# Optimization experiments

Hardware: AMD Instinct MI355X
Metric: run time of the kernel (lower is better)

Reference implementation:

```python
import jax, jax.numpy as jnp
import numpy as np

NFRAMES = 8
N_ITERS = 32        # fixed-iteration Riemannian gradient descent (geomstats FrechetMean equivalent)
EPS = 1e-7


def _l2norm(x, axis=-1):
    return x / jnp.maximum(jnp.linalg.norm(x, axis=axis, keepdims=True), EPS)


def _frechet_mean_sphere(X):
    """Batched Frechet mean on the unit hypersphere.
    X: [..., n, d] unit vectors. Returns [..., d] unit mean.
    Iteration: mu <- Exp_mu( mean_i Log_mu(x_i) ).
    """
    mu0 = _l2norm(jnp.mean(X, axis=-2))

    def step(mu, _):
        dots = jnp.clip(jnp.einsum('...d,...kd->...k', mu, X), -1.0 + 1e-6, 1.0 - 1e-6)
        theta = jnp.arccos(dots)
        safe = theta > 1e-4
        coef = jnp.where(safe, theta / jnp.sin(jnp.where(safe, theta, 1.0)), 1.0)
        # Log map: [..., n, d]
        logs = coef[..., None] * (X - dots[..., None] * mu[..., None, :])
        v = jnp.mean(logs, axis=-2)                      # tangent mean [..., d]
        vn = jnp.linalg.norm(v, axis=-1, keepdims=True)
        vsafe = vn > 1e-9
        sinc = jnp.where(vsafe, jnp.sin(vn) / jnp.where(vsafe, vn, 1.0), 1.0)
        mu_new = jnp.cos(vn) * mu + sinc * v             # Exp map
        return _l2norm(mu_new), None

    mu, _ = jax.lax.scan(step, mu0, None, length=N_ITERS)
    return mu


def setup_inputs() -> dict:
    key = jax.random.key(0)
    k1, k2 = jax.random.split(key)
    support_vecs = jax.random.normal(k1, (25, 64, NFRAMES * 2048), dtype=jnp.float32)
    target_vec = jax.random.normal(k2, (64, NFRAMES * 2048), dtype=jnp.float32)
    return {"support_vecs": support_vecs, "target_vec": target_vec}


def reference(support_vecs, target_vec):
    seqlen, bs, df = support_vecs.shape
    sup = _l2norm(support_vecs.reshape(seqlen, bs, NFRAMES, -1))   # [s,b,n,2048]
    tgt = _l2norm(target_vec.reshape(bs, NFRAMES, -1))             # [b,n,2048]
    support_means = _frechet_mean_sphere(sup)                      # [s,b,2048]
    target_means = _frechet_mean_sphere(tgt)                       # [b,2048]
    similarities = jnp.einsum('sbd,bd->sb', support_means, target_means)
    return similarities
```

## Files before the change

kernel.cpp:

```cpp
#include <hip/hip_runtime.h>
#include <math.h>

#define NFR 8
#define DD 2048
#define NS 25
#define NB 64
#define NPAIR (NS*NB)
#define NITER 32
#define WS_TGT 320000
#define SOLVE_BLKS 100

typedef __attribute__((ext_vector_type(8))) short short8;
typedef __attribute__((ext_vector_type(4))) float f32x4;

__device__ __forceinline__ float acos_fast(float x) {
    const float ax = fabsf(x);
    const bool big = ax > 0.5f;
    const float z = big ? 0.5f * (1.f - ax) : x * x;
    const float s = big ? sqrtf(z) : ax;
    float p = fmaf(z, 4.2163199048e-2f, 2.4181311049e-2f);
    p = fmaf(z, p, 4.5470025998e-2f);
    p = fmaf(z, p, 7.4953002686e-2f);
    p = fmaf(z, p, 1.6666752422e-1f);
    const float asin_s = fmaf(s * z, p, s);
    const float asin_abs = big ? (1.5707963267948966f - 2.f * asin_s) : asin_s;
    return 1.5707963267948966f - copysignf(asin_abs, x);
}

#define SPLIT2(a, b, HI, LO) { \
    const float ha_ = __uint_as_float(__float_as_uint(a) & 0xFFFF0000u); \
    const float hb_ = __uint_as_float(__float_as_uint(b) & 0xFFFF0000u); \
    HI = __builtin_amdgcn_perm(__float_as_uint(b), __float_as_uint(a), 0x07060302u); \
    LO = __builtin_amdgcn_perm(__float_as_uint((b) - hb_), __float_as_uint((a) - ha_), 0x07060302u); \
}

__device__ __forceinline__ void load_lds16(const float* g, float* l) {
    __builtin_amdgcn_global_load_lds(
        (const __attribute__((address_space(1))) void*)g,
        (__attribute__((address_space(3))) void*)l, 16, 0, 0);
}

__global__ __launch_bounds__(512) void gram_kernel(const float* __restrict__ sup,
                                                   const float* __restrict__ tgt,
                                                   float* __restrict__ ws) {
    const int bid = blockIdx.x;
    const int xcd = bid & 7;
    const int q   = bid >> 3;
    const int b   = xcd * 8 + (q & 7);
    const int sq  = q >> 3;
    const int s   = sq % NS;
    const int kh  = sq / NS;
    const int p   = s * NB + b;
    const int tid = threadIdx.x;
    const int wv  = tid >> 6;
    const int l   = tid & 63;
    const int row = l & 15;
    const int kg  = l >> 4;

    __shared__ float lds[16384];

    #pragma unroll
    for (int i = 0; i < 2; ++i) {
        const int r  = 2 * wv + i;
        const int r7 = r & 7;
        const float* g = (r < 8)
            ? sup + ((size_t)p * NFR + r) * DD + kh * 1024
            : tgt + ((size_t)b * NFR + (r - 8)) * DD + kh * 1024;
        const float* gl = g + (size_t)((l ^ r7) * 4);
        float* d = lds + r * 1024;
        #pragma unroll
        for (int c = 0; c < 4; ++c)
            load_lds16(gl + c * 256, d + c * 256);
    }
    __syncthreads();

    f32x4 accA = {0.f, 0.f, 0.f, 0.f};
    f32x4 accB = {0.f, 0.f, 0.f, 0.f};
    const int swz = (row & 7) << 4;
    const char* rowbase = (const char*)lds + row * 4096;
    #pragma unroll
    for (int st = 0; st < 4; ++st) {
        const int o0 = (wv * 128 + st * 32) * 4 + kg * 32;
        const float4 f0 = *(const float4*)(rowbase + (o0 ^ swz));
        const float4 f1 = *(const float4*)(rowbase + ((o0 + 16) ^ swz));
        union { unsigned int u[4]; short8 s8; } H, L;
        SPLIT2(f0.x, f0.y, H.u[0], L.u[0]);
        SPLIT2(f0.z, f0.w, H.u[1], L.u[1]);
        SPLIT2(f1.x, f1.y, H.u[2], L.u[2]);
        SPLIT2(f1.z, f1.w, H.u[3], L.u[3]);
        accA = __builtin_amdgcn_mfma_f32_16x16x32_bf16(H.s8, H.s8, accA, 0, 0, 0);
        accB = __builtin_amdgcn_mfma_f32_16x16x32_bf16(H.s8, L.s8, accB, 0, 0, 0);
        accB = __builtin_amdgcn_mfma_f32_16x16x32_bf16(L.s8, H.s8, accB, 0, 0, 0);
    }
    __syncthreads();

    float* part = lds;
    #pragma unroll
    for (int r = 0; r < 4; ++r)
        part[wv * 272 + (kg * 4 + r) * 17 + row] = accA[r] + accB[r];
    __syncthreads();

    if (tid < 256) {
        const int rr = tid >> 4, cc = tid & 15;
        float v = 0.f;
        #pragma unroll
        for (int w = 0; w < 8; ++w) v += part[w * 272 + rr * 17 + cc];
        if (rr < 8) {
            if (cc >= 8)
                ws[(size_t)(p * 2 + kh) * 100 + 36 + rr * 8 + (cc - 8)] = v;
            else if (cc >= rr)
                ws[(size_t)(p * 2 + kh) * 100 + rr * 8 + cc - rr * (rr + 1) / 2] = v;
        } else if (s == 0 && cc >= rr) {
            const int i8 = rr - 8, j8 = cc - 8;
            ws[WS_TGT + (size_t)(b * 2 + kh) * 36 + i8 * 8 + j8 - i8 * (i8 + 1) / 2] = v;
        }
    }
}

__global__ __launch_bounds__(256) void solve_kernel(const float* __restrict__ ws,
                                                    float* __restrict__ out) {
    const int bid = blockIdx.x;
    const int tid = threadIdx.x;
    __shared__ float synth[16 * 256];

    for (int e = tid; e < 4096; e += 256) {
        const int pp = e >> 8, ij = e & 255;
        const int i = ij >> 4, j = ij & 15;
        const int p = bid * 16 + pp;
        const int b = p & (NB - 1);
        float v = 0.f;
        if (i < 8) {
            if (j < 8) {
                const int ii = i < j ? i : j, jj = i < j ? j : i;
                const int t36 = ii*8 + jj - ii*(ii+1)/2;
                v = ws[(size_t)(p*2+0)*100 + t36] + ws[(size_t)(p*2+1)*100 + t36];
            } else {
                const int c64 = 36 + i*8 + (j-8);
                v = ws[(size_t)(p*2+0)*100 + c64] + ws[(size_t)(p*2+1)*100 + c64];
            }
        } else if (j >= 8) {
            const int i8 = i - 8, j8 = j - 8;
            const int ii = i8 < j8 ? i8 : j8, jj = i8 < j8 ? j8 : i8;
            const int t36 = ii*8 + jj - ii*(ii+1)/2;
            v = ws[WS_TGT + (size_t)(b*2+0)*36 + t36] + ws[WS_TGT + (size_t)(b*2+1)*36 + t36];
        }
        synth[e] = v;
    }
    __syncthreads();

    const int pp = tid >> 4;
    const int t16 = tid & 15;
    const int p = bid * 16 + pp;
    const float* graw = synth + pp * 256;
    const int j = t16 & 7;
    const int base = t16 & 8;
    const int R = base + j;
    const int cb = base;

    const float invn_own = rsqrtf(fmaxf(graw[R * 16 + R], 1e-14f));
    float Grow[8];
    #pragma unroll
    for (int k = 0; k < 8; ++k) {
        const float invk = rsqrtf(fmaxf(graw[(cb + k) * 16 + (cb + k)], 1e-14f));
        Grow[k] = graw[R * 16 + cb + k] * invn_own * invk;
    }

    float rs = 0.f;
    #pragma unroll
    for (int k = 0; k < 8; ++k) rs += Grow[k];
    rs += __shfl_xor(rs, 1, 8);
    rs += __shfl_xor(rs, 2, 8);
    rs += __shfl_xor(rs, 4, 8);
    float a_own = rsqrtf(fmaxf(rs, 6.4e-13f));
    float aAll[8];
    #pragma unroll
    for (int k = 0; k < 8; ++k) aAll[k] = a_own;

    for (int it = 0; it < NITER; ++it) {
        float dot = 0.f;
        #pragma unroll
        for (int k = 0; k < 8; ++k) dot = fmaf(Grow[k], aAll[k], dot);
        dot = fminf(fmaxf(dot, -1.f + 1e-6f), 1.f - 1e-6f);
        const float theta = acos_fast(dot);
        const float q = fmaf(-dot, dot, 1.0f);
        const float coef = (theta > 1e-4f) ? theta * rsqrtf(q) : 1.f;
        const float w = 0.125f * coef;
        float wAll[8];
        #pragma unroll
        for (int k = 0; k < 8; ++k) wAll[k] = __shfl(w, base + k, 16);
        float Gw = 0.f;
        #pragma unroll
        for (int k = 0; k < 8; ++k) Gw = fmaf(Grow[k], wAll[k], Gw);
        float u1 = a_own * Gw, u2 = w * Gw;
        u1 += __shfl_xor(u1, 1, 8);  u2 += __shfl_xor(u2, 1, 8);
        u1 += __shfl_xor(u1, 2, 8);  u2 += __shfl_xor(u2, 2, 8);
        u1 += __shfl_xor(u1, 4, 8);  u2 += __shfl_xor(u2, 4, 8);
        const float cdavg = u1;
        const float vnsq = fmaxf(u2 - cdavg * cdavg, 0.f);
        const float vn = sqrtf(vnsq);
        const float rev = vn * 0.15915494309189535f;
        const float sinv = __builtin_amdgcn_sinf(rev);
        const float cosv = __builtin_amdgcn_cosf(rev);
        const float sinc = (vn > 1e-9f) ? sinv / vn : 1.f;
        const float cn2 = fmaf(sinc * sinc, vnsq, cosv * cosv);
        const float rn = rsqrtf(fmaxf(cn2, 1e-14f));
        a_own = (cosv * a_own + sinc * fmaf(-cdavg, a_own, w)) * rn;
        #pragma unroll
        for (int k = 0; k < 8; ++k)
            aAll[k] = (cosv * aAll[k] + sinc * fmaf(-cdavg, aAll[k], wAll[k])) * rn;
    }

    const float ahat = a_own * invn_own;
    float at[8];
    #pragma unroll
    for (int q2 = 0; q2 < 8; ++q2) at[q2] = __shfl(ahat, 8 + q2, 16);
    float tacc = 0.f;
    #pragma unroll
    for (int q2 = 0; q2 < 8; ++q2) tacc = fmaf(graw[j * 16 + 8 + q2], at[q2], tacc);
    float sim = ahat * tacc;
    sim += __shfl_xor(sim, 1, 8);
    sim += __shfl_xor(sim, 2, 8);
    sim += __shfl_xor(sim, 4, 8);
    if (t16 == 0) out[p] = sim;
}

extern "C" void kernel_launch(void* const* d_in, const int* in_sizes, int n_in,
                              void* d_out, int out_size, void* d_ws, size_t ws_size,
                              hipStream_t stream) {
    const float* sup = (const float*)d_in[0];
    const float* tgt = (const float*)d_in[1];
    float* ws = (float*)d_ws;
    float* out = (float*)d_out;
    gram_kernel<<<NPAIR * 2, 512, 0, stream>>>(sup, tgt, ws);
    solve_kernel<<<SOLVE_BLKS, 256, 0, stream>>>(ws, out);
}
```

Measured before the change: 53.10 us.

## Pipeline support loads across seqlen slices with triple-buffered LDS in gram kernel

```diff
diff --git a/kernel.cpp b/kernel.cpp
--- a/kernel.cpp
+++ b/kernel.cpp
@@ -7,7 +7,7 @@
 #define NB 64
 #define NPAIR (NS*NB)
 #define NITER 32
-#define WS_TGT 320000
+#define WS_TGT 640000
 #define SOLVE_BLKS 100
 
 typedef __attribute__((ext_vector_type(8))) short short8;
@@ -44,76 +44,101 @@
                                                    const float* __restrict__ tgt,
                                                    float* __restrict__ ws) {
     const int bid = blockIdx.x;
-    const int xcd = bid & 7;
-    const int q   = bid >> 3;
-    const int b   = xcd * 8 + (q & 7);
-    const int sq  = q >> 3;
-    const int s   = sq % NS;
-    const int kh  = sq / NS;
-    const int p   = s * NB + b;
+    const int u   = bid >> 3;
+    const int b   = (bid & 7) * 8 + (u & 7);
+    const int u2  = u >> 3;
+    const int kq  = u2 & 3;
+    const int sg  = u2 >> 2;
     const int tid = threadIdx.x;
     const int wv  = tid >> 6;
     const int l   = tid & 63;
-    const int row = l & 15;
+    const int fr  = l & 15;
     const int kg  = l >> 4;
 
-    __shared__ float lds[16384];
-
-    #pragma unroll
-    for (int i = 0; i < 2; ++i) {
-        const int r  = 2 * wv + i;
-        const int r7 = r & 7;
-        const float* g = (r < 8)
-            ? sup + ((size_t)p * NFR + r) * DD + kh * 1024
-            : tgt + ((size_t)b * NFR + (r - 8)) * DD + kh * 1024;
-        const float* gl = g + (size_t)((l ^ r7) * 4);
-        float* d = lds + r * 1024;
-        #pragma unroll
-        for (int c = 0; c < 4; ++c)
-            load_lds16(gl + c * 256, d + c * 256);
-    }
-    __syncthreads();
-
-    f32x4 accA = {0.f, 0.f, 0.f, 0.f};
-    f32x4 accB = {0.f, 0.f, 0.f, 0.f};
-    const int swz = (row & 7) << 4;
-    const char* rowbase = (const char*)lds + row * 4096;
-    #pragma unroll
-    for (int st = 0; st < 4; ++st) {
-        const int o0 = (wv * 128 + st * 32) * 4 + kg * 32;
-        const float4 f0 = *(const float4*)(rowbase + (o0 ^ swz));
-        const float4 f1 = *(const float4*)(rowbase + ((o0 + 16) ^ swz));
-        union { unsigned int u[4]; short8 s8; } H, L;
-        SPLIT2(f0.x, f0.y, H.u[0], L.u[0]);
-        SPLIT2(f0.z, f0.w, H.u[1], L.u[1]);
-        SPLIT2(f1.x, f1.y, H.u[2], L.u[2]);
-        SPLIT2(f1.z, f1.w, H.u[3], L.u[3]);
-        accA = __builtin_amdgcn_mfma_f32_16x16x32_bf16(H.s8, H.s8, accA, 0, 0, 0);
-        accB = __builtin_amdgcn_mfma_f32_16x16x32_bf16(H.s8, L.s8, accB, 0, 0, 0);
-        accB = __builtin_amdgcn_mfma_f32_16x16x32_bf16(L.s8, H.s8, accB, 0, 0, 0);
-    }
-    __syncthreads();
-
-    float* part = lds;
-    #pragma unroll
-    for (int r = 0; r < 4; ++r)
-        part[wv * 272 + (kg * 4 + r) * 17 + row] = accA[r] + accB[r];
-    __syncthreads();
-
-    if (tid < 256) {
-        const int rr = tid >> 4, cc = tid & 15;
-        float v = 0.f;
-        #pragma unroll
-        for (int w = 0; w < 8; ++w) v += part[w * 272 + rr * 17 + cc];
-        if (rr < 8) {
-            if (cc >= 8)
-                ws[(size_t)(p * 2 + kh) * 100 + 36 + rr * 8 + (cc - 8)] = v;
-            else if (cc >= rr)
-                ws[(size_t)(p * 2 + kh) * 100 + rr * 8 + cc - rr * (rr + 1) / 2] = v;
-        } else if (s == 0 && cc >= rr) {
-            const int i8 = rr - 8, j8 = cc - 8;
-            ws[WS_TGT + (size_t)(b * 2 + kh) * 36 + i8 * 8 + j8 - i8 * (i8 + 1) / 2] = v;
-        }
+    __shared__ float tbuf[8 * 512];
+    __shared__ float sbuf[3][8 * 512];
+    __shared__ float part[8 * 272];
+
+    {
+        const float* g = tgt + ((size_t)b * NFR + wv) * DD + kq * 512;
+        const float* gl = g + (l ^ wv) * 4;
+        load_lds16(gl,       tbuf + wv * 512);
+        load_lds16(gl + 256, tbuf + wv * 512 + 256);
+    }
+    const int s0 = sg * 5;
+    {
+        #pragma unroll
+        for (int i = 0; i < 2; ++i) {
+            const float* g = sup + (((size_t)(s0 + i) * NB + b) * NFR + wv) * DD + kq * 512;
+            const float* gl = g + (l ^ wv) * 4;
+            load_lds16(gl,       sbuf[i] + wv * 512);
+            load_lds16(gl + 256, sbuf[i] + wv * 512 + 256);
+        }
+    }
+
+    #pragma unroll
+    for (int i = 0; i < 5; ++i) {
+        if (i + 2 <= 4) {
+            const int sl = (i + 2) % 3;
+            const float* g = sup + (((size_t)(s0 + i + 2) * NB + b) * NFR + wv) * DD + kq * 512;
+            const float* gl = g + (l ^ wv) * 4;
+            load_lds16(gl,       sbuf[sl] + wv * 512);
+            load_lds16(gl + 256, sbuf[sl] + wv * 512 + 256);
+        }
+        if (i <= 2)      asm volatile("s_waitcnt vmcnt(4)" ::: "memory");
+        else if (i == 3) asm volatile("s_waitcnt vmcnt(2)" ::: "memory");
+        else             asm volatile("s_waitcnt vmcnt(0)" ::: "memory");
+        __builtin_amdgcn_s_barrier();
+        __builtin_amdgcn_sched_barrier(0);
+
+        f32x4 accA = {0.f, 0.f, 0.f, 0.f};
+        f32x4 accB = {0.f, 0.f, 0.f, 0.f};
+        const char* rb = (const char*)((fr < 8) ? (sbuf[i % 3] + fr * 512)
+                                                : (tbuf + (fr - 8) * 512));
+        const int swz = (fr & 7) << 4;
+        #pragma unroll
+        for (int ch = 0; ch < 2; ++ch) {
+            const int o  = wv * 256 + ch * 128 + kg * 32;
+            const int oa = (o & 0xC00) | ((o & 0x3FF) ^ swz);
+            const int ob = ((o + 16) & 0xC00) | (((o + 16) & 0x3FF) ^ swz);
+            const float4 f0 = *(const float4*)(rb + oa);
+            const float4 f1 = *(const float4*)(rb + ob);
+            union { unsigned int u[4]; short8 s8; } H, L;
+            SPLIT2(f0.x, f0.y, H.u[0], L.u[0]);
+            SPLIT2(f0.z, f0.w, H.u[1], L.u[1]);
+            SPLIT2(f1.x, f1.y, H.u[2], L.u[2]);
+            SPLIT2(f1.z, f1.w, H.u[3], L.u[3]);
+            accA = __builtin_amdgcn_mfma_f32_16x16x32_bf16(H.s8, H.s8, accA, 0, 0, 0);
+            accB = __builtin_amdgcn_mfma_f32_16x16x32_bf16(H.s8, L.s8, accB, 0, 0, 0);
+            accB = __builtin_amdgcn_mfma_f32_16x16x32_bf16(L.s8, H.s8, accB, 0, 0, 0);
+        }
+
+        #pragma unroll
+        for (int r = 0; r < 4; ++r)
+            part[wv * 272 + (kg * 4 + r) * 17 + fr] = accA[r] + accB[r];
+        asm volatile("s_waitcnt lgkmcnt(0)" ::: "memory");
+        __builtin_amdgcn_s_barrier();
+        __builtin_amdgcn_sched_barrier(0);
+
+        if (tid < 256) {
+            const int rr = tid >> 4, cc = tid & 15;
+            float v = 0.f;
+            #pragma unroll
+            for (int w = 0; w < 8; ++w) v += part[w * 272 + rr * 17 + cc];
+            const size_t p4 = (size_t)(((s0 + i) * NB + b) * 4 + kq);
+            if (rr < 8) {
+                if (cc >= 8)
+                    ws[p4 * 100 + 36 + rr * 8 + (cc - 8)] = v;
+                else if (cc >= rr)
+                    ws[p4 * 100 + rr * 8 + cc - rr * (rr + 1) / 2] = v;
+            } else if (sg == 0 && i == 0 && cc >= rr) {
+                const int i8 = rr - 8, j8 = cc - 8;
+                ws[WS_TGT + (size_t)(b * 4 + kq) * 36 + i8 * 8 + j8 - i8 * (i8 + 1) / 2] = v;
+            }
+        }
+        asm volatile("s_waitcnt lgkmcnt(0)" ::: "memory");
+        __builtin_amdgcn_s_barrier();
+        __builtin_amdgcn_sched_barrier(0);
     }
 }
 
@@ -133,16 +158,18 @@
             if (j < 8) {
                 const int ii = i < j ? i : j, jj = i < j ? j : i;
                 const int t36 = ii*8 + jj - ii*(ii+1)/2;
-                v = ws[(size_t)(p*2+0)*100 + t36] + ws[(size_t)(p*2+1)*100 + t36];
+                #pragma unroll
+                for (int kq = 0; kq < 4; ++kq) v += ws[(size_t)(p*4+kq)*100 + t36];
             } else {
-                const int c64 = 36 + i*8 + (j-8);
-                v = ws[(size_t)(p*2+0)*100 + c64] + ws[(size_t)(p*2+1)*100 + c64];
+                #pragma unroll
+                for (int kq = 0; kq < 4; ++kq) v += ws[(size_t)(p*4+kq)*100 + 36 + i*8 + (j-8)];
             }
         } else if (j >= 8) {
             const int i8 = i - 8, j8 = j - 8;
             const int ii = i8 < j8 ? i8 : j8, jj = i8 < j8 ? j8 : i8;
             const int t36 = ii*8 + jj - ii*(ii+1)/2;
-            v = ws[WS_TGT + (size_t)(b*2+0)*36 + t36] + ws[WS_TGT + (size_t)(b*2+1)*36 + t36];
+            #pragma unroll
+            for (int kq = 0; kq < 4; ++kq) v += ws[WS_TGT + (size_t)(b*4+kq)*36 + t36];
         }
         synth[e] = v;
     }
@@ -231,6 +258,6 @@
     const float* tgt = (const float*)d_in[1];
     float* ws = (float*)d_ws;
     float* out = (float*)d_out;
-    gram_kernel<<<NPAIR * 2, 512, 0, stream>>>(sup, tgt, ws);
+    gram_kernel<<<NB * 4 * 5, 512, 0, stream>>>(sup, tgt, ws);
     solve_kernel<<<SOLVE_BLKS, 256, 0, stream>>>(ws, out);
 }
```

After: 53.49 us. No clear change (+0.7%).

## Share target rows across four support slices and split K into eight chunks

Applied to the files above, without the earlier changes.

```diff
diff --git a/kernel.cpp b/kernel.cpp
--- a/kernel.cpp
+++ b/kernel.cpp
@@ -7,7 +7,7 @@
 #define NB 64
 #define NPAIR (NS*NB)
 #define NITER 32
-#define WS_TGT 320000
+#define WS_TGT 1280000
 #define SOLVE_BLKS 100
 
 typedef __attribute__((ext_vector_type(8))) short short8;
@@ -44,76 +44,86 @@
                                                    const float* __restrict__ tgt,
                                                    float* __restrict__ ws) {
     const int bid = blockIdx.x;
-    const int xcd = bid & 7;
-    const int q   = bid >> 3;
-    const int b   = xcd * 8 + (q & 7);
-    const int sq  = q >> 3;
-    const int s   = sq % NS;
-    const int kh  = sq / NS;
-    const int p   = s * NB + b;
+    const int b   = (bid & 7) * 8 + ((bid >> 3) & 7);
+    const int u   = bid >> 6;
+    const int q   = u >> 3;
+    const int ko  = u & 7;
     const int tid = threadIdx.x;
     const int wv  = tid >> 6;
     const int l   = tid & 63;
-    const int row = l & 15;
+    const int fr  = l & 15;
     const int kg  = l >> 4;
 
-    __shared__ float lds[16384];
-
-    #pragma unroll
-    for (int i = 0; i < 2; ++i) {
-        const int r  = 2 * wv + i;
-        const int r7 = r & 7;
-        const float* g = (r < 8)
-            ? sup + ((size_t)p * NFR + r) * DD + kh * 1024
-            : tgt + ((size_t)b * NFR + (r - 8)) * DD + kh * 1024;
-        const float* gl = g + (size_t)((l ^ r7) * 4);
-        float* d = lds + r * 1024;
-        #pragma unroll
-        for (int c = 0; c < 4; ++c)
-            load_lds16(gl + c * 256, d + c * 256);
+    __shared__ float rows[40 * 256];
+    __shared__ float part[8 * 272];
+
+    #pragma unroll
+    for (int i = 0; i < 5; ++i) {
+        const int r = wv * 5 + i;
+        const float* g;
+        if (r < 8) {
+            g = tgt + ((size_t)b * NFR + r) * DD + ko * 256;
+        } else {
+            const int j = (r - 8) >> 3, rr = (r - 8) & 7;
+            const int sj = (4 * q + j < NS) ? (4 * q + j) : (NS - 1);
+            g = sup + (((size_t)sj * NB + b) * NFR + rr) * DD + ko * 256;
+        }
+        load_lds16(g + (l ^ (r & 7)) * 4, rows + r * 256);
     }
     __syncthreads();
 
-    f32x4 accA = {0.f, 0.f, 0.f, 0.f};
-    f32x4 accB = {0.f, 0.f, 0.f, 0.f};
-    const int swz = (row & 7) << 4;
-    const char* rowbase = (const char*)lds + row * 4096;
-    #pragma unroll
-    for (int st = 0; st < 4; ++st) {
-        const int o0 = (wv * 128 + st * 32) * 4 + kg * 32;
-        const float4 f0 = *(const float4*)(rowbase + (o0 ^ swz));
-        const float4 f1 = *(const float4*)(rowbase + ((o0 + 16) ^ swz));
+    const int swz = (fr & 7) << 4;
+    const int o   = wv * 128 + kg * 32;
+    const int oa  = o ^ swz;
+    const int ob  = (o + 16) ^ swz;
+    f32x4 accA[4], accB[4];
+    #pragma unroll
+    for (int j = 0; j < 4; ++j) {
+        accA[j] = (f32x4){0.f, 0.f, 0.f, 0.f};
+        accB[j] = (f32x4){0.f, 0.f, 0.f, 0.f};
+    }
+    #pragma unroll
+    for (int j = 0; j < 4; ++j) {
+        const char* rb = (const char*)((fr < 8) ? (rows + (8 + 8 * j + fr) * 256)
+                                                : (rows + (fr - 8) * 256));
+        const float4 f0 = *(const float4*)(rb + oa);
+        const float4 f1 = *(const float4*)(rb + ob);
         union { unsigned int u[4]; short8 s8; } H, L;
         SPLIT2(f0.x, f0.y, H.u[0], L.u[0]);
         SPLIT2(f0.z, f0.w, H.u[1], L.u[1]);
         SPLIT2(f1.x, f1.y, H.u[2], L.u[2]);
         SPLIT2(f1.z, f1.w, H.u[3], L.u[3]);
-        accA = __builtin_amdgcn_mfma_f32_16x16x32_bf16(H.s8, H.s8, accA, 0, 0, 0);
-        accB = __builtin_amdgcn_mfma_f32_16x16x32_bf16(H.s8, L.s8, accB, 0, 0, 0);
-        accB = __builtin_amdgcn_mfma_f32_16x16x32_bf16(L.s8, H.s8, accB, 0, 0, 0);
-    }
-    __syncthreads();
-
-    float* part = lds;
-    #pragma unroll
-    for (int r = 0; r < 4; ++r)
-        part[wv * 272 + (kg * 4 + r) * 17 + row] = accA[r] + accB[r];
-    __syncthreads();
-
-    if (tid < 256) {
-        const int rr = tid >> 4, cc = tid & 15;
-        float v = 0.f;
-        #pragma unroll
-        for (int w = 0; w < 8; ++w) v += part[w * 272 + rr * 17 + cc];
-        if (rr < 8) {
-            if (cc >= 8)
-                ws[(size_t)(p * 2 + kh) * 100 + 36 + rr * 8 + (cc - 8)] = v;
-            else if (cc >= rr)
-                ws[(size_t)(p * 2 + kh) * 100 + rr * 8 + cc - rr * (rr + 1) / 2] = v;
-        } else if (s == 0 && cc >= rr) {
-            const int i8 = rr - 8, j8 = cc - 8;
-            ws[WS_TGT + (size_t)(b * 2 + kh) * 36 + i8 * 8 + j8 - i8 * (i8 + 1) / 2] = v;
+        accA[j] = __builtin_amdgcn_mfma_f32_16x16x32_bf16(H.s8, H.s8, accA[j], 0, 0, 0);
+        accB[j] = __builtin_amdgcn_mfma_f32_16x16x32_bf16(H.s8, L.s8, accB[j], 0, 0, 0);
+        accB[j] = __builtin_amdgcn_mfma_f32_16x16x32_bf16(L.s8, H.s8, accB[j], 0, 0, 0);
+    }
+
+    #pragma unroll
+    for (int j = 0; j < 4; ++j) {
+        #pragma unroll
+        for (int r = 0; r < 4; ++r)
+            part[wv * 272 + (kg * 4 + r) * 17 + fr] = accA[j][r] + accB[j][r];
+        __syncthreads();
+        if (tid < 256) {
+            const int rr = tid >> 4, cc = tid & 15;
+            float v = 0.f;
+            #pragma unroll
+            for (int w = 0; w < 8; ++w) v += part[w * 272 + rr * 17 + cc];
+            const int sj = (4 * q + j < NS) ? (4 * q + j) : (NS - 1);
+            const size_t slot = (size_t)((sj * NB + b) * 8 + ko);
+            if (rr < 8) {
+                if (q < 6 || j == 0) {
+                    if (cc >= 8)
+                        ws[slot * 100 + 36 + rr * 8 + (cc - 8)] = v;
+                    else if (cc >= rr)
+                        ws[slot * 100 + rr * 8 + cc - rr * (rr + 1) / 2] = v;
+                }
+            } else if (j == 0 && q == 0 && cc >= rr) {
+                const int i8 = rr - 8, j8 = cc - 8;
+                ws[WS_TGT + (size_t)(b * 8 + ko) * 36 + i8 * 8 + j8 - i8 * (i8 + 1) / 2] = v;
+            }
         }
+        __syncthreads();
     }
 }
 
@@ -133,16 +143,18 @@
             if (j < 8) {
                 const int ii = i < j ? i : j, jj = i < j ? j : i;
                 const int t36 = ii*8 + jj - ii*(ii+1)/2;
-                v = ws[(size_t)(p*2+0)*100 + t36] + ws[(size_t)(p*2+1)*100 + t36];
+                #pragma unroll
+                for (int ko = 0; ko < 8; ++ko) v += ws[(size_t)(p*8+ko)*100 + t36];
             } else {
-                const int c64 = 36 + i*8 + (j-8);
-                v = ws[(size_t)(p*2+0)*100 + c64] + ws[(size_t)(p*2+1)*100 + c64];
+                #pragma unroll
+                for (int ko = 0; ko < 8; ++ko) v += ws[(size_t)(p*8+ko)*100 + 36 + i*8 + (j-8)];
             }
         } else if (j >= 8) {
             const int i8 = i - 8, j8 = j - 8;
             const int ii = i8 < j8 ? i8 : j8, jj = i8 < j8 ? j8 : i8;
             const int t36 = ii*8 + jj - ii*(ii+1)/2;
-            v = ws[WS_TGT + (size_t)(b*2+0)*36 + t36] + ws[WS_TGT + (size_t)(b*2+1)*36 + t36];
+            #pragma unroll
+            for (int ko = 0; ko < 8; ++ko) v += ws[WS_TGT + (size_t)(b*8+ko)*36 + t36];
         }
         synth[e] = v;
     }
@@ -182,8 +194,8 @@
         for (int k = 0; k < 8; ++k) dot = fmaf(Grow[k], aAll[k], dot);
         dot = fminf(fmaxf(dot, -1.f + 1e-6f), 1.f - 1e-6f);
         const float theta = acos_fast(dot);
-        const float q = fmaf(-dot, dot, 1.0f);
-        const float coef = (theta > 1e-4f) ? theta * rsqrtf(q) : 1.f;
+        const float qq = fmaf(-dot, dot, 1.0f);
+        const float coef = (theta > 1e-4f) ? theta * rsqrtf(qq) : 1.f;
         const float w = 0.125f * coef;
         float wAll[8];
         #pragma unroll
@@ -231,6 +243,6 @@
     const float* tgt = (const float*)d_in[1];
     float* ws = (float*)d_ws;
     float* out = (float*)d_out;
-    gram_kernel<<<NPAIR * 2, 512, 0, stream>>>(sup, tgt, ws);
+    gram_kernel<<<8 * 8 * 56, 512, 0, stream>>>(sup, tgt, ws);
     solve_kernel<<<SOLVE_BLKS, 256, 0, stream>>>(ws, out);
 }
```

After: 57.18 us. 7.7% more time.
